# Performance work log

Hardware: AMD Instinct MI355X
Metric: run time of the kernel (lower is better)

Reference implementation:

```python
import jax, jax.numpy as jnp
import numpy as np

B, T, IN_DIM, D, H, F, L = 16, 64, 128, 512, 8, 2048, 4  # T == DATA_ROUNDS_PER_GAME
HD = D // H
SCALE = 1.0 / np.sqrt(HD)
NEG = -1e9


def setup_inputs() -> dict:
    key = jax.random.key(0)
    ks = jax.random.split(key, 10)
    s = lambda k, shape, fan: (jax.random.normal(k, shape, jnp.float32) * (fan ** -0.5)).astype(jnp.float32)
    return {
        "x": jax.random.normal(ks[0], (B, T, IN_DIM), jnp.float32),
        "fc_w": s(ks[1], (IN_DIM, D), IN_DIM), "fc_b": jnp.zeros((D,), jnp.float32),
        "w_qkv": s(ks[2], (L, D, 3 * D), D), "b_qkv": jnp.zeros((L, 3 * D), jnp.float32),
        "w_o": s(ks[3], (L, D, D), D), "b_o": jnp.zeros((L, D), jnp.float32),
        "ln1_g": jnp.ones((L, D), jnp.float32), "ln1_b": jnp.zeros((L, D), jnp.float32),
        "w_ff1": s(ks[4], (L, D, F), D), "b_ff1": jnp.zeros((L, F), jnp.float32),
        "w_ff2": s(ks[5], (L, F, D), F), "b_ff2": jnp.zeros((L, D), jnp.float32),
        "ln2_g": jnp.ones((L, D), jnp.float32), "ln2_b": jnp.zeros((L, D), jnp.float32),
        "cls_w1": s(ks[6], (D, D // 2), D), "cls_b1": jnp.zeros((D // 2,), jnp.float32),
        "cls_w2": s(ks[7], (D // 2, 2), D // 2), "cls_b2": jnp.zeros((2,), jnp.float32),
    }


def _ln(x, g, b, eps=1e-5):
    m = x.mean(-1, keepdims=True)
    v = ((x - m) ** 2).mean(-1, keepdims=True)
    return (x - m) * jax.lax.rsqrt(v + eps) * g + b


def _encoder(h, bias, w_qkv, b_qkv, w_o, b_o, ln1_g, ln1_b, w_ff1, b_ff1, w_ff2, b_ff2, ln2_g, ln2_b):
    # post-norm TransformerEncoderLayer (PyTorch default), dropout=0
    for l in range(L):
        Bh, Th = h.shape[0], h.shape[1]
        qkv = h @ w_qkv[l] + b_qkv[l]                      # [B,T,3D]
        q, k, v = jnp.split(qkv, 3, axis=-1)
        q = q.reshape(Bh, Th, H, HD)
        k = k.reshape(Bh, Th, H, HD)
        v = v.reshape(Bh, Th, H, HD)
        scores = jnp.einsum('bqhd,bkhd->bhqk', q, k) * SCALE + bias
        attn = jax.nn.softmax(scores, axis=-1)
        o = jnp.einsum('bhqk,bkhd->bqhd', attn, v).reshape(Bh, Th, D)
        h = _ln(h + o @ w_o[l] + b_o[l], ln1_g[l], ln1_b[l])
        ff = jax.nn.relu(h @ w_ff1[l] + b_ff1[l]) @ w_ff2[l] + b_ff2[l]
        h = _ln(h + ff, ln2_g[l], ln2_b[l])
    return h


def reference(x, fc_w, fc_b, w_qkv, b_qkv, w_o, b_o, ln1_g, ln1_b, w_ff1, b_ff1,
              w_ff2, b_ff2, ln2_g, ln2_b, cls_w1, cls_b1, cls_w2, cls_b2):
    h0 = jax.nn.relu(x @ fc_w + fc_b)                       # [B,T,D]

    def per_prefix(i):
        # keys restricted to positions <= i reproduces re-running the encoder
        # on the prefix x[:, :i+1]; we read position i (the prefix's last token).
        keep = jnp.arange(T) <= i
        bias = jnp.where(keep, 0.0, NEG).astype(h0.dtype)[None, None, None, :]  # [1,1,1,T]
        out = _encoder(h0, bias, w_qkv, b_qkv, w_o, b_o, ln1_g, ln1_b,
                       w_ff1, b_ff1, w_ff2, b_ff2, ln2_g, ln2_b)
        return jnp.take(out, i, axis=1)                     # [B,D]

    y = jax.vmap(per_prefix)(jnp.arange(T))                 # [T,B,D]
    y = jnp.transpose(y, (1, 0, 2))                         # [B,T,D]
    z = jax.nn.relu(y @ cls_w1 + cls_b1) @ cls_w2 + cls_b2  # [B,T,2]
    return jax.nn.log_softmax(z, axis=-1)
```

## Files before the change

kernel.cpp:

```cpp
#include <hip/hip_runtime.h>
#include <math.h>

using u16 = unsigned short;
using u32 = unsigned int;

constexpr int Bc = 16;
constexpr int Tc = 64;
constexpr int INc = 128;
constexpr int Dc = 512;
constexpr int Hc = 8;
constexpr int Fc = 2048;
constexpr int Lc = 4;
constexpr float SCALEc = 0.125f;

constexpr int NGc = 2;
constexpr int g_p0[NGc]   = {0, 44};
constexpr int g_np[NGc]   = {44, 20};
constexpr int g_start[NGc]= {0, 18432};
constexpr int g_M[NGc]    = {18432, 18432};
constexpr int g_M3[NGc]   = {768, 384};
constexpr int g_doff[NGc] = {0, 704};
constexpr int GMAXc = 18432;
constexpr int DALLc = 1024;
constexpr int DPADc = 1152;
constexpr int VTSc  = GMAXc + 64;

typedef __attribute__((ext_vector_type(8))) short bf16x8;
typedef __attribute__((ext_vector_type(4))) float f32x4;

__device__ __forceinline__ int rowbase(int p) {
  const int q = p >> 3, r = p & 7;
  return 128 * (4 * q * (q + 1) + r * (q + 1));
}

__device__ __forceinline__ float bf2f(u16 u) {
  union { u32 i; float f; } c; c.i = (u32)u << 16; return c.f;
}
__device__ __forceinline__ u16 f2bf(float f) {
  union { float f; u32 u; } c{f};
  u32 r = (c.u + 0x7fffu + ((c.u >> 16) & 1u)) >> 16;
  return (u16)r;
}

template<bool RELU>
__global__ __launch_bounds__(256) void gemm_kernel(
    const float* __restrict__ A, const float* __restrict__ W,
    const float* __restrict__ bias, float* __restrict__ C,
    u16* __restrict__ Cb, int M, int K, int N)
{
  __shared__ float As[128][17];
  __shared__ float Ws[16][64];
  const int tid = threadIdx.x;
  const int tx = tid & 15, ty = tid >> 4;
  const int row0 = blockIdx.y * 128, col0 = blockIdx.x * 64;
  float acc[8][4];
#pragma unroll
  for (int i = 0; i < 8; ++i)
#pragma unroll
    for (int j = 0; j < 4; ++j) acc[i][j] = 0.f;
  const int ar = tid >> 1, ak = (tid & 1) * 8;
  const int wr = tid >> 4, wc = (tid & 15) * 4;
  for (int k0 = 0; k0 < K; k0 += 16) {
    const float* ap = A + (size_t)(row0 + ar) * K + k0 + ak;
    float4 a0 = *(const float4*)ap;
    float4 a1 = *(const float4*)(ap + 4);
    As[ar][ak+0]=a0.x; As[ar][ak+1]=a0.y; As[ar][ak+2]=a0.z; As[ar][ak+3]=a0.w;
    As[ar][ak+4]=a1.x; As[ar][ak+5]=a1.y; As[ar][ak+6]=a1.z; As[ar][ak+7]=a1.w;
    *(float4*)&Ws[wr][wc] = *(const float4*)(W + (size_t)(k0 + wr) * N + col0 + wc);
    __syncthreads();
#pragma unroll
    for (int kk = 0; kk < 16; ++kk) {
      const float4 w4 = *(const float4*)&Ws[kk][tx * 4];
#pragma unroll
      for (int i = 0; i < 8; ++i) {
        const float av = As[ty + 16 * i][kk];
        acc[i][0] += av * w4.x; acc[i][1] += av * w4.y;
        acc[i][2] += av * w4.z; acc[i][3] += av * w4.w;
      }
    }
    __syncthreads();
  }
#pragma unroll
  for (int i = 0; i < 8; ++i) {
    const int r = row0 + ty + 16 * i, c = col0 + tx * 4;
    float4 v;
    v.x = acc[i][0] + bias[c+0]; v.y = acc[i][1] + bias[c+1];
    v.z = acc[i][2] + bias[c+2]; v.w = acc[i][3] + bias[c+3];
    if (RELU) { v.x=fmaxf(v.x,0.f); v.y=fmaxf(v.y,0.f); v.z=fmaxf(v.z,0.f); v.w=fmaxf(v.w,0.f); }
    *(float4*)&C[(size_t)r * N + c] = v;
    uint2 pk;
    pk.x = (u32)f2bf(v.x) | ((u32)f2bf(v.y) << 16);
    pk.y = (u32)f2bf(v.z) | ((u32)f2bf(v.w) << 16);
    *(uint2*)&Cb[(size_t)r * N + c] = pk;
  }
}

__global__ __launch_bounds__(256) void transpose_conv4(
    const float* __restrict__ src0, u16* __restrict__ dst0, int K, int N,
    size_t sstride, size_t dstride)
{
  const float* src = src0 + (size_t)blockIdx.z * sstride;
  u16* dst = dst0 + (size_t)blockIdx.z * dstride;
  __shared__ float t[32][33];
  const int bx = blockIdx.x * 32;
  const int by = blockIdx.y * 32;
  const int x = threadIdx.x, y = threadIdx.y;
#pragma unroll
  for (int i = 0; i < 32; i += 8) t[y + i][x] = src[(size_t)(by + y + i) * N + bx + x];
  __syncthreads();
#pragma unroll
  for (int i = 0; i < 32; i += 8)
    dst[(size_t)(bx + y + i) * K + by + x] = f2bf(t[x][y + i]);
}

__global__ __launch_bounds__(256) void transpose_v(
    const u16* __restrict__ qkvsrc, u16* __restrict__ vt, int vstride)
{
  __shared__ u16 t[64][65];
  const int r0 = blockIdx.x * 64;
  const int d0 = blockIdx.y * 64;
  const int tid = threadIdx.x;
  const int rr = tid >> 2, cc = (tid & 3) * 16;
  const u16* src = qkvsrc + (size_t)(r0 + rr) * 1536 + 1024 + d0 + cc;
  union { uint4 v; u16 s[8]; } ua, ub;
  ua.v = *(const uint4*)src;
  ub.v = *(const uint4*)(src + 8);
#pragma unroll
  for (int i = 0; i < 8; ++i) { t[rr][cc + i] = ua.s[i]; t[rr][cc + 8 + i] = ub.s[i]; }
  __syncthreads();
  const int dd = tid >> 2, kk = (tid & 3) * 16;
  union { uint4 v; u16 s[8]; } w0, w1;
#pragma unroll
  for (int i = 0; i < 8; ++i) { w0.s[i] = t[kk + i][dd]; w1.s[i] = t[kk + 8 + i][dd]; }
  u16* dst = vt + (size_t)(d0 + dd) * vstride + r0 + kk;
  *(uint4*)dst = w0.v;
  *(uint4*)(dst + 8) = w1.v;
}

__device__ __forceinline__ void stage_tile(const u16* __restrict__ src, int ldk, u16* lds)
{
  const int tid = threadIdx.x;
#pragma unroll
  for (int q = 0; q < 4; ++q) {
    const int p16 = tid + (q << 8);
    const int row = p16 >> 3;
    const int s   = p16 & 7;
    const int k16 = s ^ (row & 7);
    const u16* g = src + (size_t)row * ldk + (k16 << 3);
    __builtin_amdgcn_global_load_lds(
        (const __attribute__((address_space(1))) void*)g,
        (__attribute__((address_space(3))) void*)(lds + (p16 << 3)),
        16, 0, 0);
  }
}

__device__ __forceinline__ void stage_tile64(const u16* __restrict__ src, int ldk, u16* lds)
{
  const int tid = threadIdx.x;
#pragma unroll
  for (int q = 0; q < 2; ++q) {
    const int p16 = tid + (q << 8);
    const int row = p16 >> 3;
    const int s   = p16 & 7;
    const int k16 = s ^ (row & 7);
    const u16* g = src + (size_t)row * ldk + (k16 << 3);
    __builtin_amdgcn_global_load_lds(
        (const __attribute__((address_space(1))) void*)g,
        (__attribute__((address_space(3))) void*)(lds + (p16 << 3)),
        16, 0, 0);
  }
}

template<bool RELU, bool OUT_BF16>
__global__ __launch_bounds__(256) void gemm_mfma(
    const u16* __restrict__ A, const u16* __restrict__ Wt,
    const float* __restrict__ bias, void* __restrict__ Cout,
    int M, int K, int N)
{
  __shared__ u16 As[2][128 * 64];
  __shared__ u16 Bs[2][128 * 64];

  const int tid  = threadIdx.x;
  const int lane = tid & 63;
  const int wave = tid >> 6;
  const int wr = wave >> 1;
  const int wc = wave & 1;

  const int gx = gridDim.x;
  const int nwg = gx * gridDim.y;
  const int lin = blockIdx.y * gx + blockIdx.x;
  const int qq = nwg >> 3, r8 = nwg & 7;
  const int xcd = lin & 7, pos = lin >> 3;
  const int orig = (xcd < r8) ? (xcd * (qq + 1) + pos)
                              : (r8 * (qq + 1) + (xcd - r8) * qq + pos);
  const int row0 = (orig / gx) * 128;
  const int col0 = (orig % gx) * 128;

  f32x4 acc[4][4];
#pragma unroll
  for (int i = 0; i < 4; ++i)
#pragma unroll
    for (int j = 0; j < 4; ++j) acc[i][j] = f32x4{0.f, 0.f, 0.f, 0.f};

  const int nk = K >> 6;
  const int arow = wr * 64 + (lane & 15);
  const int brow = wc * 64 + (lane & 15);
  const int kq   = lane >> 4;

  stage_tile(A  + (size_t)row0 * K, K, &As[0][0]);
  stage_tile(Wt + (size_t)col0 * K, K, &Bs[0][0]);

  for (int t = 0; t < nk; ++t) {
    const int cur = t & 1;
    if (t + 1 < nk) {
      const int k0 = (t + 1) << 6;
      stage_tile(A  + (size_t)row0 * K + k0, K, &As[cur ^ 1][0]);
      stage_tile(Wt + (size_t)col0 * K + k0, K, &Bs[cur ^ 1][0]);
      asm volatile("s_waitcnt vmcnt(8)\n\ts_barrier" ::: "memory");
    } else {
      asm volatile("s_waitcnt vmcnt(0)\n\ts_barrier" ::: "memory");
    }
    const u16* Ab = &As[cur][0];
    const u16* Bb = &Bs[cur][0];
#pragma unroll
    for (int kk = 0; kk < 2; ++kk) {
      bf16x8 af[4], bfr[4];
      const int c = kk * 4 + kq;
#pragma unroll
      for (int i = 0; i < 4; ++i) {
        const int ra = arow + i * 16;
        af[i]  = *reinterpret_cast<const bf16x8*>(Ab + ra * 64 + ((c ^ (ra & 7)) << 3));
        const int rb = brow + i * 16;
        bfr[i] = *reinterpret_cast<const bf16x8*>(Bb + rb * 64 + ((c ^ (rb & 7)) << 3));
      }
#pragma unroll
      for (int mi = 0; mi < 4; ++mi)
#pragma unroll
        for (int ni = 0; ni < 4; ++ni)
          acc[mi][ni] = __builtin_amdgcn_mfma_f32_16x16x32_bf16(af[mi], bfr[ni], acc[mi][ni], 0, 0, 0);
    }
    asm volatile("s_barrier" ::: "memory");
  }

  const int r0 = row0 + wr * 64 + ((lane >> 4) << 2);
  const int c0 = col0 + wc * 64 + (lane & 15);
#pragma unroll
  for (int mi = 0; mi < 4; ++mi)
#pragma unroll
    for (int ni = 0; ni < 4; ++ni) {
      const int col = c0 + ni * 16;
      const float bsv = bias[col];
#pragma unroll
      for (int j = 0; j < 4; ++j) {
        const int row = r0 + mi * 16 + j;
        float o = acc[mi][ni][j] + bsv;
        if (RELU) o = fmaxf(o, 0.f);
        if (OUT_BF16) ((u16*)Cout)[(size_t)row * N + col] = f2bf(o);
        else          ((float*)Cout)[(size_t)row * N + col] = o;
      }
    }
}

template<bool RELU, bool OUT_BF16>
__global__ __launch_bounds__(256) void gemm_mfma_n64(
    const u16* __restrict__ A, const u16* __restrict__ Wt,
    const float* __restrict__ bias, void* __restrict__ Cout,
    int M, int K, int N)
{
  __shared__ u16 As[2][128 * 64];
  __shared__ u16 Bs[2][64 * 64];

  const int tid  = threadIdx.x;
  const int lane = tid & 63;
  const int wave = tid >> 6;

  const int gx = gridDim.x;
  const int nwg = gx * gridDim.y;
  const int lin = blockIdx.y * gx + blockIdx.x;
  const int qq = nwg >> 3, r8 = nwg & 7;
  const int xcd = lin & 7, pos = lin >> 3;
  const int orig = (xcd < r8) ? (xcd * (qq + 1) + pos)
                              : (r8 * (qq + 1) + (xcd - r8) * qq + pos);
  const int row0 = (orig / gx) * 128;
  const int col0 = (orig % gx) * 64;

  f32x4 acc[2][4];
#pragma unroll
  for (int i = 0; i < 2; ++i)
#pragma unroll
    for (int j = 0; j < 4; ++j) acc[i][j] = f32x4{0.f, 0.f, 0.f, 0.f};

  const int nk = K >> 6;
  const int arow = wave * 32 + (lane & 15);
  const int brow = lane & 15;
  const int kq   = lane >> 4;

  stage_tile  (A  + (size_t)row0 * K, K, &As[0][0]);
  stage_tile64(Wt + (size_t)col0 * K, K, &Bs[0][0]);

  for (int t = 0; t < nk; ++t) {
    const int cur = t & 1;
    if (t + 1 < nk) {
      const int k0 = (t + 1) << 6;
      stage_tile  (A  + (size_t)row0 * K + k0, K, &As[cur ^ 1][0]);
      stage_tile64(Wt + (size_t)col0 * K + k0, K, &Bs[cur ^ 1][0]);
      asm volatile("s_waitcnt vmcnt(6)\n\ts_barrier" ::: "memory");
    } else {
      asm volatile("s_waitcnt vmcnt(0)\n\ts_barrier" ::: "memory");
    }
    const u16* Ab = &As[cur][0];
    const u16* Bb = &Bs[cur][0];
#pragma unroll
    for (int kk = 0; kk < 2; ++kk) {
      bf16x8 af[2], bfr[4];
      const int c = kk * 4 + kq;
#pragma unroll
      for (int i = 0; i < 2; ++i) {
        const int ra = arow + i * 16;
        af[i] = *reinterpret_cast<const bf16x8*>(Ab + ra * 64 + ((c ^ (ra & 7)) << 3));
      }
#pragma unroll
      for (int i = 0; i < 4; ++i) {
        const int rb = brow + i * 16;
        bfr[i] = *reinterpret_cast<const bf16x8*>(Bb + rb * 64 + ((c ^ (rb & 7)) << 3));
      }
#pragma unroll
      for (int mi = 0; mi < 2; ++mi)
#pragma unroll
        for (int ni = 0; ni < 4; ++ni)
          acc[mi][ni] = __builtin_amdgcn_mfma_f32_16x16x32_bf16(af[mi], bfr[ni], acc[mi][ni], 0, 0, 0);
    }
    asm volatile("s_barrier" ::: "memory");
  }

  const int r0 = row0 + wave * 32 + ((lane >> 4) << 2);
  const int c0 = col0 + (lane & 15);
#pragma unroll
  for (int mi = 0; mi < 2; ++mi)
#pragma unroll
    for (int ni = 0; ni < 4; ++ni) {
      const int col = c0 + ni * 16;
      const float bsv = bias[col];
#pragma unroll
      for (int j = 0; j < 4; ++j) {
        const int row = r0 + mi * 16 + j;
        float o = acc[mi][ni][j] + bsv;
        if (RELU) o = fmaxf(o, 0.f);
        if (OUT_BF16) ((u16*)Cout)[(size_t)row * N + col] = f2bf(o);
        else          ((float*)Cout)[(size_t)row * N + col] = o;
      }
    }
}

template<bool SHARED>
__global__ __launch_bounds__(64) void attn_mfma_kernel(
    const u16* __restrict__ qkv, const u16* __restrict__ vt, int vstride,
    u16* __restrict__ attno, int p0, int gstart)
{
  const int hh = blockIdx.x, b = blockIdx.y, p = p0 + blockIdx.z;
  const int NT = p + 1;
  const int NT8 = (NT + 7) & ~7;
  const int rb = rowbase(p) + b * NT8 - gstart;
  const int sb = SHARED ? (b * 64) : rb;
  const int tid = threadIdx.x;
  const int lc = tid & 15, lg = tid >> 4;

  __shared__ u16 Plds[64][72];
  __shared__ u16 VTl[4096];
  __shared__ float invl[64];

  {
    const u16* vbase = vt + (size_t)(hh * 64) * vstride + sb;
#pragma unroll
    for (int it = 0; it < 8; ++it) {
      const int gi = tid + (it << 6);
      const int dd = gi >> 3, s = gi & 7;
      const u16* src = vbase + (size_t)dd * vstride + ((s ^ (dd & 7)) << 3);
      __builtin_amdgcn_global_load_lds(
          (const __attribute__((address_space(1))) void*)src,
          (__attribute__((address_space(3))) void*)(&VTl[gi << 3]), 16, 0, 0);
    }
  }

  f32x4 st[4][4];
#pragma unroll
  for (int i = 0; i < 4; ++i)
#pragma unroll
    for (int j = 0; j < 4; ++j) st[i][j] = f32x4{0.f, 0.f, 0.f, 0.f};

#pragma unroll
  for (int kt = 0; kt < 2; ++kt) {
    bf16x8 kf[4], qf[4];
#pragma unroll
    for (int t = 0; t < 4; ++t) {
      if (t * 16 < NT) {
        const size_t rbase = (size_t)(sb + t * 16 + lc) * 1536 + hh * 64 + kt * 32 + lg * 8;
        qf[t] = *reinterpret_cast<const bf16x8*>(qkv + rbase);
        kf[t] = *reinterpret_cast<const bf16x8*>(qkv + rbase + 512);
      }
    }
#pragma unroll
    for (int mi = 0; mi < 4; ++mi)
      if (mi * 16 < NT)
#pragma unroll
        for (int ni = 0; ni < 4; ++ni)
          if (ni * 16 < NT)
            st[mi][ni] = __builtin_amdgcn_mfma_f32_16x16x32_bf16(kf[mi], qf[ni], st[mi][ni], 0, 0, 0);
  }

#pragma unroll
  for (int ni = 0; ni < 4; ++ni) {
    float mm = -3.0e38f;
#pragma unroll
    for (int mi = 0; mi < 4; ++mi)
#pragma unroll
      for (int e = 0; e < 4; ++e)
        if (16 * mi + 4 * lg + e < NT) mm = fmaxf(mm, st[mi][ni][e]);
    mm = fmaxf(mm, __shfl_xor(mm, 16));
    mm = fmaxf(mm, __shfl_xor(mm, 32));
    float ss = 0.f;
#pragma unroll
    for (int mi = 0; mi < 4; ++mi) {
      u16 pb[4];
#pragma unroll
      for (int e = 0; e < 4; ++e) {
        const float pe = (16 * mi + 4 * lg + e < NT)
                           ? __expf((st[mi][ni][e] - mm) * SCALEc) : 0.f;
        ss += pe;
        pb[e] = f2bf(pe);
      }
      uint2 pk;
      pk.x = (u32)pb[0] | ((u32)pb[1] << 16);
      pk.y = (u32)pb[2] | ((u32)pb[3] << 16);
      *reinterpret_cast<uint2*>(&Plds[16 * ni + lc][16 * mi + 4 * lg]) = pk;
    }
    ss += __shfl_xor(ss, 16);
    ss += __shfl_xor(ss, 32);
    if (lg == 0) invl[16 * ni + lc] = 1.f / ss;
  }

  asm volatile("s_waitcnt vmcnt(0)" ::: "memory");
  __syncthreads();

  f32x4 oc[4][4];
#pragma unroll
  for (int i = 0; i < 4; ++i)
#pragma unroll
    for (int j = 0; j < 4; ++j) oc[i][j] = f32x4{0.f, 0.f, 0.f, 0.f};

#pragma unroll
  for (int kt = 0; kt < 2; ++kt) {
    if (kt * 32 < NT) {
      bf16x8 pa[4], vbf[4];
#pragma unroll
      for (int t = 0; t < 4; ++t) {
        if (t * 16 < NT)
          pa[t] = *reinterpret_cast<const bf16x8*>(&Plds[t * 16 + lc][kt * 32 + lg * 8]);
        const int dd = t * 16 + lc;
        vbf[t] = *reinterpret_cast<const bf16x8*>(
            &VTl[dd * 64 + (((4 * kt + lg) ^ (lc & 7)) << 3)]);
      }
#pragma unroll
      for (int qt = 0; qt < 4; ++qt)
        if (qt * 16 < NT)
#pragma unroll
          for (int dt = 0; dt < 4; ++dt)
            oc[qt][dt] = __builtin_amdgcn_mfma_f32_16x16x32_bf16(pa[qt], vbf[dt], oc[qt][dt], 0, 0, 0);
    }
  }

#pragma unroll
  for (int qt = 0; qt < 4; ++qt) {
    if (qt * 16 < NT) {
#pragma unroll
      for (int e = 0; e < 4; ++e) {
        const int qrow = qt * 16 + 4 * lg + e;
        if (qrow < NT) {
          const float inv = invl[qrow];
          u16* dst = attno + (size_t)(rb + qrow) * Dc + hh * 64 + lc;
#pragma unroll
          for (int dt = 0; dt < 4; ++dt)
            dst[dt * 16] = f2bf(oc[qt][dt][e] * inv);
        }
      }
    }
  }
}

__global__ __launch_bounds__(64) void attn_diag_kernel(
    const u16* __restrict__ kv3, const u16* __restrict__ qd,
    u16* __restrict__ attno_d, int p0, int gstart, int doff)
{
  const int hh = blockIdx.x, b = blockIdx.y, pl = blockIdx.z;
  const int p = p0 + pl;
  const int NT = p + 1;
  const int NT8 = (NT + 7) & ~7;
  const int rb = rowbase(p) + b * NT8 - gstart;
  const int tid = threadIdx.x;
  const int rd = doff + pl * 16 + b;

  __shared__ u16 Ks[64][64];
  __shared__ u16 Vs[64][64];

  const int lrow = tid >> 3;
  const int lc8  = tid & 7;
  for (int t0 = 0; t0 < NT; t0 += 8) {
    const int tr = rb + t0 + lrow;
    const int csrc = (lc8 ^ lrow) << 3;
    const u16* gk = kv3 + (size_t)tr * 1024 + hh * 64 + csrc;
    const u16* gv = kv3 + (size_t)tr * 1024 + 512 + hh * 64 + csrc;
    __builtin_amdgcn_global_load_lds(
        (const __attribute__((address_space(1))) void*)gk,
        (__attribute__((address_space(3))) void*)(&Ks[t0][0] + tid * 8), 16, 0, 0);
    __builtin_amdgcn_global_load_lds(
        (const __attribute__((address_space(1))) void*)gv,
        (__attribute__((address_space(3))) void*)(&Vs[t0][0] + tid * 8), 16, 0, 0);
  }

  const u16* qp = qd + (size_t)rd * Dc + hh * 64;
  float qv[64];
#pragma unroll
  for (int c8 = 0; c8 < 8; ++c8) {
    const bf16x8 q8 = *reinterpret_cast<const bf16x8*>(qp + c8 * 8);
#pragma unroll
    for (int i = 0; i < 8; ++i) qv[c8 * 8 + i] = bf2f((u16)q8[i]);
  }
  asm volatile("s_waitcnt vmcnt(0)" ::: "memory");
  __syncthreads();

  float dot = -1e30f;
  if (tid < NT) {
    dot = 0.f;
#pragma unroll
    for (int c8 = 0; c8 < 8; ++c8) {
      const bf16x8 k8 = *reinterpret_cast<const bf16x8*>(
          &Ks[tid][0] + ((c8 ^ (tid & 7)) << 3));
#pragma unroll
      for (int i = 0; i < 8; ++i) dot += qv[c8 * 8 + i] * bf2f((u16)k8[i]);
    }
    dot *= SCALEc;
  }
  float mm = dot;
#pragma unroll
  for (int off = 32; off; off >>= 1) mm = fmaxf(mm, __shfl_xor(mm, off));
  const float pt = __expf(dot - mm);
  float s = pt;
#pragma unroll
  for (int off = 32; off; off >>= 1) s += __shfl_xor(s, off);
  const float inv = 1.f / s;

  float o = 0.f;
  for (int t = 0; t < NT; ++t) {
    const float ptt = __shfl(pt, t);
    o += ptt * bf2f(Vs[t][(((tid >> 3) ^ (t & 7)) << 3) + (tid & 7)]);
  }
  attno_d[(size_t)rd * Dc + hh * 64 + tid] = f2bf(o * inv);
}

__device__ inline float wave_sum(float v) {
#pragma unroll
  for (int off = 32; off; off >>= 1) v += __shfl_xor(v, off);
  return v;
}

__global__ __launch_bounds__(256) void res_ln_kernel(
    u16* __restrict__ hb, const u16* __restrict__ tmpb,
    const float* __restrict__ g, const float* __restrict__ bt)
{
  const size_t row = (size_t)blockIdx.x * 4 + (threadIdx.x >> 6);
  const int t = threadIdx.x & 63;
  float v[8];
  float s = 0.f;
#pragma unroll
  for (int i = 0; i < 8; ++i) {
    v[i] = bf2f(hb[row * Dc + i * 64 + t]) + bf2f(tmpb[row * Dc + i * 64 + t]);
    s += v[i];
  }
  s = wave_sum(s);
  const float mean = s * (1.f / 512.f);
  float vs = 0.f;
#pragma unroll
  for (int i = 0; i < 8; ++i) { const float d = v[i] - mean; vs += d * d; }
  vs = wave_sum(vs);
  const float rstd = rsqrtf(vs * (1.f / 512.f) + 1e-5f);
#pragma unroll
  for (int i = 0; i < 8; ++i)
    hb[row * Dc + i * 64 + t] =
        f2bf((v[i] - mean) * rstd * g[i * 64 + t] + bt[i * 64 + t]);
}

__global__ __launch_bounds__(64) void res_ln0_kernel(
    const u16* __restrict__ h0b, u16* __restrict__ hb,
    const u16* __restrict__ tmpb, const float* __restrict__ g,
    const float* __restrict__ bt, int p0, int gstart)
{
  const int t = blockIdx.x, b = blockIdx.y, p = p0 + blockIdx.z;
  if (t > p) return;
  const int NT8 = (p + 8) & ~7;
  const size_t row = (size_t)(rowbase(p) + b * NT8 + t - gstart);
  const int tt = threadIdx.x;
  const u16* src = h0b + (size_t)(b * 64 + t) * Dc;
  float v[8];
  float s = 0.f;
#pragma unroll
  for (int i = 0; i < 8; ++i) {
    v[i] = bf2f(src[i * 64 + tt]) + bf2f(tmpb[row * Dc + i * 64 + tt]);
    s += v[i];
  }
  s = wave_sum(s);
  const float mean = s * (1.f / 512.f);
  float vs = 0.f;
#pragma unroll
  for (int i = 0; i < 8; ++i) { const float d = v[i] - mean; vs += d * d; }
  vs = wave_sum(vs);
  const float rstd = rsqrtf(vs * (1.f / 512.f) + 1e-5f);
#pragma unroll
  for (int i = 0; i < 8; ++i)
    hb[row * Dc + i * 64 + tt] =
        f2bf((v[i] - mean) * rstd * g[i * 64 + tt] + bt[i * 64 + tt]);
}

__global__ __launch_bounds__(128) void gather_diag(
    const u16* __restrict__ hb, u16* __restrict__ hbd,
    int p0, int gstart, int doff)
{
  const int pl = blockIdx.x >> 4, b = blockIdx.x & 15;
  const int p = p0 + pl;
  const int NT8 = (p + 8) & ~7;
  const size_t src = (size_t)(rowbase(p) + b * NT8 + p - gstart);
  ((uint2*)(hbd + (size_t)(doff + blockIdx.x) * Dc))[threadIdx.x] =
      ((const uint2*)(hb + src * Dc))[threadIdx.x];
}

__global__ __launch_bounds__(256) void cls_kernel(
    const u16* __restrict__ hbd, const float* __restrict__ w1,
    const float* __restrict__ b1, const float* __restrict__ w2,
    const float* __restrict__ b2, float* __restrict__ out)
{
  const int row = blockIdx.x;
  const int b = row >> 6, p = row & 63;
  const int rd = (p < 44) ? (p * 16 + b) : (704 + (p - 44) * 16 + b);
  const int j = threadIdx.x;
  __shared__ float ys[512];
  ys[j]       = bf2f(hbd[(size_t)rd * Dc + j]);
  ys[j + 256] = bf2f(hbd[(size_t)rd * Dc + 256 + j]);
  __syncthreads();

  float acc = b1[j];
  for (int d = 0; d < 512; ++d) acc += ys[d] * w1[(size_t)d * 256 + j];
  acc = fmaxf(acc, 0.f);

  float c0 = acc * w2[j * 2 + 0];
  float c1 = acc * w2[j * 2 + 1];
  c0 = wave_sum(c0);
  c1 = wave_sum(c1);

  __shared__ float r0[4], r1[4];
  const int w = j >> 6, lane = j & 63;
  if (lane == 0) { r0[w] = c0; r1[w] = c1; }
  __syncthreads();
  if (j == 0) {
    const float z0 = r0[0] + r0[1] + r0[2] + r0[3] + b2[0];
    const float z1 = r1[0] + r1[1] + r1[2] + r1[3] + b2[1];
    const float mz = fmaxf(z0, z1);
    const float lse = mz + logf(expf(z0 - mz) + expf(z1 - mz));
    out[row * 2 + 0] = z0 - lse;
    out[row * 2 + 1] = z1 - lse;
  }
}

extern "C" void kernel_launch(void* const* d_in, const int* in_sizes, int n_in,
                              void* d_out, int out_size, void* d_ws, size_t ws_size,
                              hipStream_t stream)
{
  if (n_in < 19) return;
  const float* x      = (const float*)d_in[0];
  const float* fc_w   = (const float*)d_in[1];
  const float* fc_b   = (const float*)d_in[2];
  const float* w_qkv  = (const float*)d_in[3];
  const float* b_qkv  = (const float*)d_in[4];
  const float* w_o    = (const float*)d_in[5];
  const float* b_o    = (const float*)d_in[6];
  const float* ln1_g  = (const float*)d_in[7];
  const float* ln1_b  = (const float*)d_in[8];
  const float* w_ff1  = (const float*)d_in[9];
  const float* b_ff1  = (const float*)d_in[10];
  const float* w_ff2  = (const float*)d_in[11];
  const float* b_ff2  = (const float*)d_in[12];
  const float* ln2_g  = (const float*)d_in[13];
  const float* ln2_b  = (const float*)d_in[14];
  const float* cls_w1 = (const float*)d_in[15];
  const float* cls_b1 = (const float*)d_in[16];
  const float* cls_w2 = (const float*)d_in[17];
  const float* cls_b2 = (const float*)d_in[18];
  float* out = (float*)d_out;

  char* wp = (char*)d_ws;
  auto alloc = [&](size_t bytes) -> char* {
    char* p = wp; wp += (bytes + 255) & ~(size_t)255; return p;
  };
  float* h0  = (float*)alloc((size_t)Bc * Tc * Dc * 4);
  u16*   h0b = (u16*)  alloc((size_t)Bc * Tc * Dc * 2);
  u16*   qkv0= (u16*)  alloc((size_t)Bc * Tc * 3 * Dc * 2);
  u16*   vt0 = (u16*)  alloc((size_t)Dc * Bc * Tc * 2);
  u16* wtqA  = (u16*)alloc((size_t)Lc * 3 * Dc * Dc * 2);
  u16* wtoA  = (u16*)alloc((size_t)Lc * Dc * Dc * 2);
  u16* wtf1A = (u16*)alloc((size_t)Lc * Fc * Dc * 2);
  u16* wtf2A = (u16*)alloc((size_t)Lc * Dc * Fc * 2);
  const size_t RS = (size_t)GMAXc + 64;
  u16*   hb    = (u16*)  alloc((size_t)GMAXc * Dc * 2);
  u16*   qkvb  = (u16*)  alloc(RS * 3 * Dc * 2);
  u16*   attno = (u16*)  alloc((size_t)GMAXc * Dc * 2);
  u16*   tmpb  = (u16*)  alloc((size_t)GMAXc * Dc * 2);
  u16*   ffb   = (u16*)  alloc((size_t)GMAXc * Fc * 2);
  u16*   vt    = (u16*)  alloc((size_t)Dc * VTSc * 2);
  u16*   hbdiag= (u16*)  alloc((size_t)DPADc * Dc * 2);
  u16*   attnd = (u16*)  alloc((size_t)DPADc * Dc * 2);
  u16*   qd    = (u16*)  alloc((size_t)DPADc * Dc * 2);
  if ((size_t)(wp - (char*)d_ws) > ws_size) return;
  u16* kv3 = qkvb;

  u16 *wtq[Lc], *wto[Lc], *wtf1[Lc], *wtf2[Lc];
  for (int l = 0; l < Lc; ++l) {
    wtq[l]  = wtqA  + (size_t)l * 3 * Dc * Dc;
    wto[l]  = wtoA  + (size_t)l * Dc * Dc;
    wtf1[l] = wtf1A + (size_t)l * Fc * Dc;
    wtf2[l] = wtf2A + (size_t)l * Dc * Fc;
  }

  const dim3 tb(32, 8);
  transpose_conv4<<<dim3(3 * Dc / 32, Dc / 32, Lc), tb, 0, stream>>>(
      w_qkv, wtqA, Dc, 3 * Dc, (size_t)Dc * 3 * Dc, (size_t)3 * Dc * Dc);
  transpose_conv4<<<dim3(Dc / 32, Dc / 32, Lc), tb, 0, stream>>>(
      w_o, wtoA, Dc, Dc, (size_t)Dc * Dc, (size_t)Dc * Dc);
  transpose_conv4<<<dim3(Fc / 32, Dc / 32, Lc), tb, 0, stream>>>(
      w_ff1, wtf1A, Dc, Fc, (size_t)Dc * Fc, (size_t)Fc * Dc);
  transpose_conv4<<<dim3(Dc / 32, Fc / 32, Lc), tb, 0, stream>>>(
      w_ff2, wtf2A, Fc, Dc, (size_t)Fc * Dc, (size_t)Dc * Fc);

  gemm_kernel<true><<<dim3(Dc / 64, (Bc * Tc) / 128), 256, 0, stream>>>(
      x, fc_w, fc_b, h0, h0b, Bc * Tc, INc, Dc);

  gemm_mfma<false, true><<<dim3(3 * Dc / 128, (Bc * Tc) / 128), 256, 0, stream>>>(
      h0b, wtq[0], b_qkv, qkv0, Bc * Tc, Dc, 3 * Dc);
  transpose_v<<<dim3((Bc * Tc) / 64, 8), 256, 0, stream>>>(qkv0, vt0, Bc * Tc);

  for (int g = 0; g < NGc; ++g) {
    const int p0 = g_p0[g], np = g_np[g], gs = g_start[g], Mg = g_M[g];
    const int M3 = g_M3[g], doff = g_doff[g];

    attn_mfma_kernel<true><<<dim3(Hc, Bc, np), 64, 0, stream>>>(
        qkv0, vt0, Bc * Tc, attno, p0, gs);
    gemm_mfma_n64<false, true><<<dim3(Dc / 64, Mg / 128), 256, 0, stream>>>(
        attno, wto[0], b_o, tmpb, Mg, Dc, Dc);
    res_ln0_kernel<<<dim3(64, 16, np), 64, 0, stream>>>(
        h0b, hb, tmpb, ln1_g, ln1_b, p0, gs);
    gemm_mfma<true, true><<<dim3(Fc / 128, Mg / 128), 256, 0, stream>>>(
        hb, wtf1[0], b_ff1, ffb, Mg, Dc, Fc);
    gemm_mfma_n64<false, true><<<dim3(Dc / 64, Mg / 128), 256, 0, stream>>>(
        ffb, wtf2[0], b_ff2, tmpb, Mg, Fc, Dc);
    res_ln_kernel<<<Mg / 4, 256, 0, stream>>>(hb, tmpb, ln2_g, ln2_b);

    for (int l = 1; l < 3; ++l) {
      gemm_mfma<false, true><<<dim3(3 * Dc / 128, Mg / 128), 256, 0, stream>>>(
          hb, wtq[l], b_qkv + (size_t)l * 3 * Dc, qkvb, Mg, Dc, 3 * Dc);
      transpose_v<<<dim3(Mg / 64, 8), 256, 0, stream>>>(qkvb, vt, VTSc);
      attn_mfma_kernel<false><<<dim3(Hc, Bc, np), 64, 0, stream>>>(
          qkvb, vt, VTSc, attno, p0, gs);
      gemm_mfma_n64<false, true><<<dim3(Dc / 64, Mg / 128), 256, 0, stream>>>(
          attno, wto[l], b_o + (size_t)l * Dc, tmpb, Mg, Dc, Dc);
      res_ln_kernel<<<Mg / 4, 256, 0, stream>>>(hb, tmpb, ln1_g + l * Dc, ln1_b + l * Dc);
      gemm_mfma<true, true><<<dim3(Fc / 128, Mg / 128), 256, 0, stream>>>(
          hb, wtf1[l], b_ff1 + (size_t)l * Fc, ffb, Mg, Dc, Fc);
      gemm_mfma_n64<false, true><<<dim3(Dc / 64, Mg / 128), 256, 0, stream>>>(
          ffb, wtf2[l], b_ff2 + (size_t)l * Dc, tmpb, Mg, Fc, Dc);
      res_ln_kernel<<<Mg / 4, 256, 0, stream>>>(hb, tmpb, ln2_g + l * Dc, ln2_b + l * Dc);
    }

    {
      const int l = 3;
      gather_diag<<<np * 16, 128, 0, stream>>>(hb, hbdiag, p0, gs, doff);
      gemm_mfma_n64<false, true><<<dim3(Dc / 64, M3 / 128), 256, 0, stream>>>(
          hbdiag + (size_t)doff * Dc, wtq[l], b_qkv + (size_t)l * 3 * Dc,
          qd + (size_t)doff * Dc, M3, Dc, Dc);
      gemm_mfma<false, true><<<dim3(2 * Dc / 128, Mg / 128), 256, 0, stream>>>(
          hb, wtq[l] + (size_t)512 * Dc, b_qkv + (size_t)l * 3 * Dc + 512,
          kv3, Mg, Dc, 2 * Dc);
      attn_diag_kernel<<<dim3(Hc, Bc, np), 64, 0, stream>>>(
          kv3, qd, attnd, p0, gs, doff);
    }
  }

  {
    const int l = 3;
    gemm_mfma_n64<false, true><<<dim3(Dc / 64, DALLc / 128), 256, 0, stream>>>(
        attnd, wto[l], b_o + (size_t)l * Dc, tmpb, DALLc, Dc, Dc);
    res_ln_kernel<<<DALLc / 4, 256, 0, stream>>>(hbdiag, tmpb,
                                                 ln1_g + l * Dc, ln1_b + l * Dc);
    gemm_mfma<true, true><<<dim3(Fc / 128, DALLc / 128), 256, 0, stream>>>(
        hbdiag, wtf1[l], b_ff1 + (size_t)l * Fc, ffb, DALLc, Dc, Fc);
    gemm_mfma_n64<false, true><<<dim3(Dc / 64, DALLc / 128), 256, 0, stream>>>(
        ffb, wtf2[l], b_ff2 + (size_t)l * Dc, tmpb, DALLc, Fc, Dc);
    res_ln_kernel<<<DALLc / 4, 256, 0, stream>>>(hbdiag, tmpb,
                                                 ln2_g + l * Dc, ln2_b + l * Dc);
  }

  cls_kernel<<<Bc * Tc, 256, 0, stream>>>(hbdiag, cls_w1, cls_b1, cls_w2, cls_b2, out);
}
```

Baseline: 1.501 ms.

## Use MFMA GEMMs for input and classifier layers, triple-buffer n64 GEMM

```diff
diff --git a/kernel.cpp b/kernel.cpp
--- a/kernel.cpp
+++ b/kernel.cpp
@@ -42,56 +42,16 @@
   return (u16)r;
 }
 
-template<bool RELU>
-__global__ __launch_bounds__(256) void gemm_kernel(
-    const float* __restrict__ A, const float* __restrict__ W,
-    const float* __restrict__ bias, float* __restrict__ C,
-    u16* __restrict__ Cb, int M, int K, int N)
-{
-  __shared__ float As[128][17];
-  __shared__ float Ws[16][64];
-  const int tid = threadIdx.x;
-  const int tx = tid & 15, ty = tid >> 4;
-  const int row0 = blockIdx.y * 128, col0 = blockIdx.x * 64;
-  float acc[8][4];
-#pragma unroll
-  for (int i = 0; i < 8; ++i)
-#pragma unroll
-    for (int j = 0; j < 4; ++j) acc[i][j] = 0.f;
-  const int ar = tid >> 1, ak = (tid & 1) * 8;
-  const int wr = tid >> 4, wc = (tid & 15) * 4;
-  for (int k0 = 0; k0 < K; k0 += 16) {
-    const float* ap = A + (size_t)(row0 + ar) * K + k0 + ak;
-    float4 a0 = *(const float4*)ap;
-    float4 a1 = *(const float4*)(ap + 4);
-    As[ar][ak+0]=a0.x; As[ar][ak+1]=a0.y; As[ar][ak+2]=a0.z; As[ar][ak+3]=a0.w;
-    As[ar][ak+4]=a1.x; As[ar][ak+5]=a1.y; As[ar][ak+6]=a1.z; As[ar][ak+7]=a1.w;
-    *(float4*)&Ws[wr][wc] = *(const float4*)(W + (size_t)(k0 + wr) * N + col0 + wc);
-    __syncthreads();
-#pragma unroll
-    for (int kk = 0; kk < 16; ++kk) {
-      const float4 w4 = *(const float4*)&Ws[kk][tx * 4];
-#pragma unroll
-      for (int i = 0; i < 8; ++i) {
-        const float av = As[ty + 16 * i][kk];
-        acc[i][0] += av * w4.x; acc[i][1] += av * w4.y;
-        acc[i][2] += av * w4.z; acc[i][3] += av * w4.w;
-      }
-    }
-    __syncthreads();
-  }
-#pragma unroll
-  for (int i = 0; i < 8; ++i) {
-    const int r = row0 + ty + 16 * i, c = col0 + tx * 4;
-    float4 v;
-    v.x = acc[i][0] + bias[c+0]; v.y = acc[i][1] + bias[c+1];
-    v.z = acc[i][2] + bias[c+2]; v.w = acc[i][3] + bias[c+3];
-    if (RELU) { v.x=fmaxf(v.x,0.f); v.y=fmaxf(v.y,0.f); v.z=fmaxf(v.z,0.f); v.w=fmaxf(v.w,0.f); }
-    *(float4*)&C[(size_t)r * N + c] = v;
+__global__ __launch_bounds__(256) void conv_bf16(
+    const float* __restrict__ x, u16* __restrict__ xb, int n)
+{
+  const int i = (blockIdx.x * 256 + threadIdx.x) * 4;
+  if (i < n) {
+    const float4 v = *(const float4*)(x + i);
     uint2 pk;
     pk.x = (u32)f2bf(v.x) | ((u32)f2bf(v.y) << 16);
     pk.y = (u32)f2bf(v.z) | ((u32)f2bf(v.w) << 16);
-    *(uint2*)&Cb[(size_t)r * N + c] = pk;
+    *(uint2*)(xb + i) = pk;
   }
 }
 
@@ -267,8 +227,8 @@
     const float* __restrict__ bias, void* __restrict__ Cout,
     int M, int K, int N)
 {
-  __shared__ u16 As[2][128 * 64];
-  __shared__ u16 Bs[2][64 * 64];
+  __shared__ u16 As[3][128 * 64];
+  __shared__ u16 Bs[3][64 * 64];
 
   const int tid  = threadIdx.x;
   const int lane = tid & 63;
@@ -297,17 +257,24 @@
 
   stage_tile  (A  + (size_t)row0 * K, K, &As[0][0]);
   stage_tile64(Wt + (size_t)col0 * K, K, &Bs[0][0]);
-
+  if (nk > 1) {
+    stage_tile  (A  + (size_t)row0 * K + 64, K, &As[1][0]);
+    stage_tile64(Wt + (size_t)col0 * K + 64, K, &Bs[1][0]);
+  }
+
+  int cur = 0;
   for (int t = 0; t < nk; ++t) {
-    const int cur = t & 1;
     if (t + 1 < nk) {
-      const int k0 = (t + 1) << 6;
-      stage_tile  (A  + (size_t)row0 * K + k0, K, &As[cur ^ 1][0]);
-      stage_tile64(Wt + (size_t)col0 * K + k0, K, &Bs[cur ^ 1][0]);
       asm volatile("s_waitcnt vmcnt(6)\n\ts_barrier" ::: "memory");
     } else {
       asm volatile("s_waitcnt vmcnt(0)\n\ts_barrier" ::: "memory");
     }
+    if (t + 2 < nk) {
+      const int k0 = (t + 2) << 6;
+      const int nb = (t + 2) % 3;
+      stage_tile  (A  + (size_t)row0 * K + k0, K, &As[nb][0]);
+      stage_tile64(Wt + (size_t)col0 * K + k0, K, &Bs[nb][0]);
+    }
     const u16* Ab = &As[cur][0];
     const u16* Bb = &Bs[cur][0];
 #pragma unroll
@@ -330,7 +297,7 @@
         for (int ni = 0; ni < 4; ++ni)
           acc[mi][ni] = __builtin_amdgcn_mfma_f32_16x16x32_bf16(af[mi], bfr[ni], acc[mi][ni], 0, 0, 0);
     }
-    asm volatile("s_barrier" ::: "memory");
+    cur = (cur == 2) ? 0 : cur + 1;
   }
 
   const int r0 = row0 + wave * 32 + ((lane >> 4) << 2);
@@ -632,36 +599,26 @@
       ((const uint2*)(hb + src * Dc))[threadIdx.x];
 }
 
-__global__ __launch_bounds__(256) void cls_kernel(
-    const u16* __restrict__ hbd, const float* __restrict__ w1,
-    const float* __restrict__ b1, const float* __restrict__ w2,
+__global__ __launch_bounds__(64) void cls_fin_kernel(
+    const u16* __restrict__ ffc, const float* __restrict__ w2,
     const float* __restrict__ b2, float* __restrict__ out)
 {
   const int row = blockIdx.x;
   const int b = row >> 6, p = row & 63;
   const int rd = (p < 44) ? (p * 16 + b) : (704 + (p - 44) * 16 + b);
-  const int j = threadIdx.x;
-  __shared__ float ys[512];
-  ys[j]       = bf2f(hbd[(size_t)rd * Dc + j]);
-  ys[j + 256] = bf2f(hbd[(size_t)rd * Dc + 256 + j]);
-  __syncthreads();
-
-  float acc = b1[j];
-  for (int d = 0; d < 512; ++d) acc += ys[d] * w1[(size_t)d * 256 + j];
-  acc = fmaxf(acc, 0.f);
-
-  float c0 = acc * w2[j * 2 + 0];
-  float c1 = acc * w2[j * 2 + 1];
+  const int t = threadIdx.x;
+  float c0 = 0.f, c1 = 0.f;
+#pragma unroll
+  for (int k = 0; k < 4; ++k) {
+    const int j = t + k * 64;
+    const float fv = bf2f(ffc[(size_t)rd * 256 + j]);
+    c0 += fv * w2[j * 2 + 0];
+    c1 += fv * w2[j * 2 + 1];
+  }
   c0 = wave_sum(c0);
   c1 = wave_sum(c1);
-
-  __shared__ float r0[4], r1[4];
-  const int w = j >> 6, lane = j & 63;
-  if (lane == 0) { r0[w] = c0; r1[w] = c1; }
-  __syncthreads();
-  if (j == 0) {
-    const float z0 = r0[0] + r0[1] + r0[2] + r0[3] + b2[0];
-    const float z1 = r1[0] + r1[1] + r1[2] + r1[3] + b2[1];
+  if (t == 0) {
+    const float z0 = c0 + b2[0], z1 = c1 + b2[1];
     const float mz = fmaxf(z0, z1);
     const float lse = mz + logf(expf(z0 - mz) + expf(z1 - mz));
     out[row * 2 + 0] = z0 - lse;
@@ -699,7 +656,7 @@
   auto alloc = [&](size_t bytes) -> char* {
     char* p = wp; wp += (bytes + 255) & ~(size_t)255; return p;
   };
-  float* h0  = (float*)alloc((size_t)Bc * Tc * Dc * 4);
+  u16*   xb  = (u16*)  alloc((size_t)Bc * Tc * INc * 2);
   u16*   h0b = (u16*)  alloc((size_t)Bc * Tc * Dc * 2);
   u16*   qkv0= (u16*)  alloc((size_t)Bc * Tc * 3 * Dc * 2);
   u16*   vt0 = (u16*)  alloc((size_t)Dc * Bc * Tc * 2);
@@ -707,6 +664,8 @@
   u16* wtoA  = (u16*)alloc((size_t)Lc * Dc * Dc * 2);
   u16* wtf1A = (u16*)alloc((size_t)Lc * Fc * Dc * 2);
   u16* wtf2A = (u16*)alloc((size_t)Lc * Dc * Fc * 2);
+  u16* fcwt  = (u16*)alloc((size_t)Dc * INc * 2);
+  u16* w1t   = (u16*)alloc((size_t)256 * Dc * 2);
   const size_t RS = (size_t)GMAXc + 64;
   u16*   hb    = (u16*)  alloc((size_t)GMAXc * Dc * 2);
   u16*   qkvb  = (u16*)  alloc(RS * 3 * Dc * 2);
@@ -717,6 +676,7 @@
   u16*   hbdiag= (u16*)  alloc((size_t)DPADc * Dc * 2);
   u16*   attnd = (u16*)  alloc((size_t)DPADc * Dc * 2);
   u16*   qd    = (u16*)  alloc((size_t)DPADc * Dc * 2);
+  u16*   ffc   = (u16*)  alloc((size_t)DALLc * 256 * 2);
   if ((size_t)(wp - (char*)d_ws) > ws_size) return;
   u16* kv3 = qkvb;
 
@@ -737,9 +697,15 @@
       w_ff1, wtf1A, Dc, Fc, (size_t)Dc * Fc, (size_t)Fc * Dc);
   transpose_conv4<<<dim3(Dc / 32, Fc / 32, Lc), tb, 0, stream>>>(
       w_ff2, wtf2A, Fc, Dc, (size_t)Fc * Dc, (size_t)Dc * Fc);
-
-  gemm_kernel<true><<<dim3(Dc / 64, (Bc * Tc) / 128), 256, 0, stream>>>(
-      x, fc_w, fc_b, h0, h0b, Bc * Tc, INc, Dc);
+  transpose_conv4<<<dim3(Dc / 32, INc / 32, 1), tb, 0, stream>>>(
+      fc_w, fcwt, INc, Dc, 0, 0);
+  transpose_conv4<<<dim3(256 / 32, Dc / 32, 1), tb, 0, stream>>>(
+      cls_w1, w1t, Dc, 256, 0, 0);
+
+  conv_bf16<<<(Bc * Tc * INc / 4 + 255) / 256, 256, 0, stream>>>(
+      x, xb, Bc * Tc * INc);
+  gemm_mfma_n64<true, true><<<dim3(Dc / 64, (Bc * Tc) / 128), 256, 0, stream>>>(
+      xb, fcwt, fc_b, h0b, Bc * Tc, INc, Dc);
 
   gemm_mfma<false, true><<<dim3(3 * Dc / 128, (Bc * Tc) / 128), 256, 0, stream>>>(
       h0b, wtq[0], b_qkv, qkv0, Bc * Tc, Dc, 3 * Dc);
@@ -805,5 +771,7 @@
                                                  ln2_g + l * Dc, ln2_b + l * Dc);
   }
 
-  cls_kernel<<<Bc * Tc, 256, 0, stream>>>(hbdiag, cls_w1, cls_b1, cls_w2, cls_b2, out);
-}
+  gemm_mfma_n64<true, true><<<dim3(256 / 64, DALLc / 128), 256, 0, stream>>>(
+      hbdiag, w1t, cls_b1, ffc, DALLc, Dc, 256);
+  cls_fin_kernel<<<Bc * Tc, 64, 0, stream>>>(ffc, cls_w2, cls_b2, out);
+}
```

After: 1.630 ms. +8.6%, slower.
